# Optimization experiments

Hardware: AMD Instinct MI355X
Metric: run time of the kernel (lower is better)

The kernel has to match this reference:

```python
import jax, jax.numpy as jnp
import numpy as np

NUM_BLOCKS = 8
BLOCK_SIZE = 96  # 768 // 8
LAMBDA = 0.01


def softshrink(x, lam=LAMBDA):
    return jnp.sign(x) * jnp.maximum(jnp.abs(x) - lam, 0.0)


def setup_inputs() -> dict:
    key = jax.random.key(0)
    k1, k2, k3 = jax.random.split(key, 3)
    B, H, W, C = 4, 128, 128, 768
    # xavier_uniform bound for [block_size, block_size] fan_in=fan_out=96
    bound = float(np.sqrt(6.0 / (BLOCK_SIZE + BLOCK_SIZE)))
    x = jax.random.normal(k1, (B, H, W, C), dtype=jnp.float32)
    w1 = jax.random.uniform(k2, (2, NUM_BLOCKS, BLOCK_SIZE, BLOCK_SIZE), minval=-bound, maxval=bound, dtype=jnp.float32)
    w2 = jax.random.uniform(k3, (2, NUM_BLOCKS, BLOCK_SIZE, BLOCK_SIZE), minval=-bound, maxval=bound, dtype=jnp.float32)
    b1 = jnp.zeros((2, NUM_BLOCKS, BLOCK_SIZE), dtype=jnp.float32)
    b2 = jnp.zeros((2, NUM_BLOCKS, BLOCK_SIZE), dtype=jnp.float32)
    return {"x": x, "w1": w1, "w2": w2, "b1": b1, "b2": b2}


def reference(x, w1, w2, b1, b2):
    bias = x
    B, H, W, C = x.shape
    xf = jnp.fft.rfft2(x.astype(jnp.float32), axes=(1, 2), norm='ortho')  # [B,H,W//2+1,C] complex
    Wf = xf.shape[2]
    xf = xf.reshape(B, H, Wf, NUM_BLOCKS, BLOCK_SIZE)
    xr, xi = jnp.real(xf), jnp.imag(xf)
    # first complex block-diagonal MLP layer
    o1r = jnp.einsum('bhwki,kio->bhwko', xr, w1[0]) - jnp.einsum('bhwki,kio->bhwko', xi, w1[1]) + b1[0]
    o1i = jnp.einsum('bhwki,kio->bhwko', xi, w1[0]) + jnp.einsum('bhwki,kio->bhwko', xr, w1[1]) + b1[1]
    o1r = softshrink(o1r)
    o1i = softshrink(o1i)
    # second layer
    o2r = jnp.einsum('bhwki,kio->bhwko', o1r, w2[0]) - jnp.einsum('bhwki,kio->bhwko', o1i, w2[1]) + b2[0]
    o2i = jnp.einsum('bhwki,kio->bhwko', o1i, w2[0]) + jnp.einsum('bhwki,kio->bhwko', o1r, w2[1]) + b2[1]
    o2r = softshrink(o2r)
    o2i = softshrink(o2i)
    yf = (o2r + 1j * o2i).reshape(B, H, Wf, C)
    y = jnp.fft.irfft2(yf, s=(H, W), axes=(1, 2), norm='ortho')
    return y.astype(x.dtype) + bias
```

## Files before the change

kernel.cpp:

```cpp
#include <hip/hip_runtime.h>
#include <cmath>

#define PI_D 3.14159265358979323846

static constexpr int B_ = 4, H_ = 128, W_ = 128, C_ = 768, WF = 65;
static constexpr size_t PLANE = (size_t)B_ * H_ * WF * C_;
static constexpr float LAMBDA_ = 0.01f;

using short8   = __attribute__((ext_vector_type(8))) short;
using floatx16 = __attribute__((ext_vector_type(16))) float;

__device__ __forceinline__ float2 cmul(float2 a, float2 b) {
  return make_float2(a.x * b.x - a.y * b.y, a.x * b.y + a.y * b.x);
}
__device__ __forceinline__ unsigned short f2bfu(float f) {
  union { float f; unsigned u; } v; v.f = f;
  unsigned r = v.u + 0x7FFFu + ((v.u >> 16) & 1u);
  return (unsigned short)(r >> 16);
}
__device__ __forceinline__ float bf2f(unsigned short u) {
  union { unsigned u; float f; } v; v.u = (unsigned)u << 16;
  return v.f;
}
__device__ __forceinline__ float softshrink(float v) {
  return v > LAMBDA_ ? v - LAMBDA_ : (v < -LAMBDA_ ? v + LAMBDA_ : 0.0f);
}

template<int SIGN, int S>
__device__ __forceinline__ void fft64_stage(float2* z, const float2* tw) {
  constexpr int half = 1 << S;
  #pragma unroll
  for (int g = 0; g < 32; ++g) {
    const int j  = g & (half - 1);
    const int i0 = ((g >> S) << (S + 1)) + j;
    const int i1 = i0 + half;
    float2 w = tw[j << (5 - S)];
    if (SIGN > 0) w.y = -w.y;
    float2 t = cmul(w, z[i1]);
    float2 a = z[i0];
    z[i0] = make_float2(a.x + t.x, a.y + t.y);
    z[i1] = make_float2(a.x - t.x, a.y - t.y);
  }
}
template<int SIGN>
__device__ __forceinline__ void fft64(float2* z, const float2* tw) {
  #pragma unroll
  for (int i = 0; i < 64; ++i) {
    const int j = ((i >> 5) & 1) | (((i >> 4) & 1) << 1) | (((i >> 3) & 1) << 2)
                | (((i >> 2) & 1) << 3) | (((i >> 1) & 1) << 4) | ((i & 1) << 5);
    if (i < j) { float2 t = z[i]; z[i] = z[j]; z[j] = t; }
  }
  fft64_stage<SIGN, 0>(z, tw);
  fft64_stage<SIGN, 1>(z, tw);
  fft64_stage<SIGN, 2>(z, tw);
  fft64_stage<SIGN, 3>(z, tw);
  fft64_stage<SIGN, 4>(z, tw);
  fft64_stage<SIGN, 5>(z, tw);
}

__global__ void k_init_tw(float2* tw64, float2* tw128) {
  int t = threadIdx.x;
  if (t < 32) {
    double th = -2.0 * PI_D * (double)t / 64.0;
    tw64[t] = make_float2((float)cos(th), (float)sin(th));
  }
  if (t < 65) {
    double th = -PI_D * (double)t / 64.0;
    tw128[t] = make_float2((float)cos(th), (float)sin(th));
  }
}

__global__ __launch_bounds__(256) void k_wconv(
    const float* __restrict__ w1, const float* __restrict__ w2,
    unsigned short* __restrict__ wbf) {
  const int flat = blockIdx.x * 256 + threadIdx.x;
  const int i  = flat % 104;
  const int t2 = flat / 104;
  const int o  = t2 % 96;
  const int t3 = t2 / 96;
  const int ri = t3 & 1;
  const int t4 = t3 >> 1;
  const int kb = t4 & 7;
  const int layer = t4 >> 3;
  const float* w = layer ? w2 : w1;
  unsigned short v = 0;
  if (i < 96) v = f2bfu(w[((size_t)(ri * 8 + kb) * 96 + i) * 96 + o]);
  wbf[flat] = v;
}

__global__ __launch_bounds__(256) void k_rfft_w(
    const float* __restrict__ x,
    unsigned short* __restrict__ Sr, unsigned short* __restrict__ Si,
    const float2* __restrict__ tw64g, const float2* __restrict__ tw128g) {
  __shared__ float2 stw64[32];
  __shared__ float2 stw128[65];
  const int tid = threadIdx.x;
  if (tid < 32) stw64[tid]  = tw64g[tid];
  if (tid < 65) stw128[tid] = tw128g[tid];
  __syncthreads();
  const int blk = blockIdx.x;
  const int cc = blk % 3, bh = blk / 3;
  const int c = cc * 256 + tid;
  const float* xp = x + (size_t)bh * (W_ * C_) + c;
  float2 z[64];
  #pragma unroll
  for (int n = 0; n < 64; ++n) {
    z[n].x = xp[(size_t)(2 * n) * C_];
    z[n].y = xp[(size_t)(2 * n + 1) * C_];
  }
  fft64<-1>(z, stw64);
  const size_t obase = (size_t)bh * (WF * C_) + c;
  #pragma unroll
  for (int k = 0; k <= 64; ++k) {
    float2 a  = z[k & 63];
    float2 bq = z[(64 - k) & 63];
    float2 ze = make_float2(0.5f * (a.x + bq.x), 0.5f * (a.y - bq.y));
    float2 d  = make_float2(0.5f * (a.x - bq.x), 0.5f * (a.y + bq.y));
    float2 zo = make_float2(d.y, -d.x);
    float2 w  = stw128[k];
    float2 X  = make_float2(ze.x + w.x * zo.x - w.y * zo.y,
                            ze.y + w.x * zo.y + w.y * zo.x);
    Sr[obase + (size_t)k * C_] = f2bfu(X.x);
    Si[obase + (size_t)k * C_] = f2bfu(X.y);
  }
}

template<int SIGN>
__global__ __launch_bounds__(128) void k_fft_h(
    unsigned short* __restrict__ Sr, unsigned short* __restrict__ Si,
    const float2* __restrict__ tw64g, const float2* __restrict__ tw128g) {
  __shared__ float2 stw64[32];
  __shared__ float2 stw128[65];
  __shared__ float2 Elds[64][64];
  const int tid = threadIdx.x;
  if (tid < 32) stw64[tid]  = tw64g[tid];
  if (tid < 65) stw128[tid] = tw128g[tid];
  __syncthreads();
  const int half = tid >> 6, lane = tid & 63;
  const int blk = blockIdx.x;
  const int cc = blk % 12;
  const int t2 = blk / 12;
  const int wf = t2 % 65, b = t2 / 65;
  const int c = cc * 64 + lane;
  const size_t base = ((size_t)b * (H_ * WF) + wf) * C_ + c;
  const size_t hstr = (size_t)WF * C_;
  float2 z[64];
  #pragma unroll
  for (int n = 0; n < 64; ++n) {
    const size_t a = base + (size_t)(2 * n + half) * hstr;
    z[n].x = bf2f(Sr[a]); z[n].y = bf2f(Si[a]);
  }
  fft64<SIGN>(z, stw64);
  if (half == 0) {
    #pragma unroll
    for (int k = 0; k < 64; ++k) Elds[k][lane] = z[k];
  } else {
    #pragma unroll
    for (int k = 0; k < 64; ++k) {
      float2 w = stw128[k];
      if (SIGN > 0) w.y = -w.y;
      z[k] = cmul(w, z[k]);
    }
  }
  __syncthreads();
  if (half == 1) {
    const float scale = (SIGN < 0) ? (1.0f / 128.0f) : 1.0f;
    #pragma unroll
    for (int k = 0; k < 64; ++k) {
      float2 E = Elds[k][lane];
      float2 t = z[k];
      const size_t a0 = base + (size_t)k * hstr;
      const size_t a1 = base + (size_t)(k + 64) * hstr;
      Sr[a0] = f2bfu((E.x + t.x) * scale); Si[a0] = f2bfu((E.y + t.y) * scale);
      Sr[a1] = f2bfu((E.x - t.x) * scale); Si[a1] = f2bfu((E.y - t.y) * scale);
    }
  }
}

__global__ __launch_bounds__(256) void k_mlp(
    unsigned short* __restrict__ Sr, unsigned short* __restrict__ Si,
    const unsigned short* __restrict__ wbf,
    const float* __restrict__ b1, const float* __restrict__ b2) {
  __shared__ __align__(16) unsigned short smem[32768];
  unsigned short* wr   = smem;
  unsigned short* wi   = smem + 9984;
  unsigned short* obuf = smem + 19968;
  const int tid = threadIdx.x;
  const int kb  = blockIdx.x & 7;
  const int p0  = (blockIdx.x >> 3) * 64;
  const int wv  = tid >> 6, lane = tid & 63;
  const int mh = wv & 1, nh = wv >> 1;
  const int n32 = lane & 31, khalf = lane >> 5;

  {
    const unsigned short* g = wbf + (size_t)kb * 19968;
    #pragma unroll
    for (int it = 0; it < 10; ++it) {
      int idx = tid + it * 256;
      if (idx < 2496) *(short8*)&smem[idx * 8] = *(const short8*)&g[idx * 8];
    }
  }
  __syncthreads();

  floatx16 acc[3];
  #pragma unroll
  for (int t = 0; t < 3; ++t)
    #pragma unroll
    for (int e = 0; e < 16; ++e) acc[t][e] = 0.0f;

  const size_t arow = (size_t)(p0 + mh * 32 + n32) * C_ + kb * 96;
  #pragma unroll
  for (int kk = 0; kk < 12; ++kk) {
    const int kr = kk >= 6;
    const int kloc = (kk - kr * 6) * 16 + khalf * 8;
    const unsigned short* ap = (kr ? Si : Sr) + arow + kloc;
    short8 afr = *(const short8*)ap;
    const unsigned short* bb = (kr != nh) ? wi : wr;
    #pragma unroll
    for (int nt = 0; nt < 3; ++nt) {
      short8 bfr = *(const short8*)&bb[(nt * 32 + n32) * 104 + kloc];
      if (kr && !nh) {
        union { short8 s; int v[4]; } u; u.s = bfr;
        u.v[0] ^= 0x80008000; u.v[1] ^= 0x80008000;
        u.v[2] ^= 0x80008000; u.v[3] ^= 0x80008000;
        bfr = u.s;
      }
      acc[nt] = __builtin_amdgcn_mfma_f32_32x32x16_bf16(afr, bfr, acc[nt], 0, 0, 0);
    }
  }

  #pragma unroll
  for (int nt = 0; nt < 3; ++nt) {
    const int o = nt * 32 + n32;
    const float bs = b1[(nh * 8 + kb) * 96 + o];
    const int n = nh * 96 + o;
    #pragma unroll
    for (int reg = 0; reg < 16; ++reg) {
      const int m = mh * 32 + (reg & 3) + 8 * (reg >> 2) + 4 * khalf;
      obuf[m * 200 + n] = f2bfu(softshrink(acc[nt][reg] + bs));
    }
  }
  __syncthreads();

  {
    const unsigned short* g = wbf + (size_t)(8 + kb) * 19968;
    #pragma unroll
    for (int it = 0; it < 10; ++it) {
      int idx = tid + it * 256;
      if (idx < 2496) *(short8*)&smem[idx * 8] = *(const short8*)&g[idx * 8];
    }
  }
  __syncthreads();

  #pragma unroll
  for (int t = 0; t < 3; ++t)
    #pragma unroll
    for (int e = 0; e < 16; ++e) acc[t][e] = 0.0f;

  const int arow2 = (mh * 32 + n32) * 200;
  #pragma unroll
  for (int kk = 0; kk < 12; ++kk) {
    const int kr = kk >= 6;
    const int klocW = (kk - kr * 6) * 16 + khalf * 8;
    short8 afr = *(const short8*)&obuf[arow2 + kk * 16 + khalf * 8];
    const unsigned short* bb = (kr != nh) ? wi : wr;
    #pragma unroll
    for (int nt = 0; nt < 3; ++nt) {
      short8 bfr = *(const short8*)&bb[(nt * 32 + n32) * 104 + klocW];
      if (kr && !nh) {
        union { short8 s; int v[4]; } u; u.s = bfr;
        u.v[0] ^= 0x80008000; u.v[1] ^= 0x80008000;
        u.v[2] ^= 0x80008000; u.v[3] ^= 0x80008000;
        bfr = u.s;
      }
      acc[nt] = __builtin_amdgcn_mfma_f32_32x32x16_bf16(afr, bfr, acc[nt], 0, 0, 0);
    }
  }

  unsigned short* plane = nh ? Si : Sr;
  #pragma unroll
  for (int nt = 0; nt < 3; ++nt) {
    const int o = nt * 32 + n32;
    const float bs = b2[(nh * 8 + kb) * 96 + o];
    #pragma unroll
    for (int reg = 0; reg < 16; ++reg) {
      const int m = mh * 32 + (reg & 3) + 8 * (reg >> 2) + 4 * khalf;
      plane[(size_t)(p0 + m) * C_ + kb * 96 + o] = f2bfu(softshrink(acc[nt][reg] + bs));
    }
  }
}

__global__ __launch_bounds__(256) void k_irfft_w(
    const unsigned short* __restrict__ Sr, const unsigned short* __restrict__ Si,
    const float* __restrict__ xin, float* __restrict__ y,
    const float2* __restrict__ tw64g, const float2* __restrict__ tw128g) {
  __shared__ float2 stw64[32];
  __shared__ float2 stw128[65];
  const int tid = threadIdx.x;
  if (tid < 32) stw64[tid]  = tw64g[tid];
  if (tid < 65) stw128[tid] = tw128g[tid];
  __syncthreads();
  const int blk = blockIdx.x;
  const int cc = blk % 3, bh = blk / 3;
  const int c = cc * 256 + tid;
  const size_t ibase = (size_t)bh * (WF * C_) + c;
  float2 z[64];
  {
    float x0r  = bf2f(Sr[ibase]);
    float x64r = bf2f(Sr[ibase + (size_t)64 * C_]);
    z[0] = make_float2(0.5f * (x0r + x64r), 0.5f * (x0r - x64r));
  }
  #pragma unroll
  for (int k = 1; k <= 32; ++k) {
    float2 a, b;
    a.x = bf2f(Sr[ibase + (size_t)k * C_]);        a.y = bf2f(Si[ibase + (size_t)k * C_]);
    b.x = bf2f(Sr[ibase + (size_t)(64 - k) * C_]); b.y = bf2f(Si[ibase + (size_t)(64 - k) * C_]);
    float2 s = make_float2(0.5f * (a.x + b.x), 0.5f * (a.y - b.y));
    float2 d = make_float2(0.5f * (a.x - b.x), 0.5f * (a.y + b.y));
    float2 w = stw128[k]; w.y = -w.y;
    float2 zo = cmul(w, d);
    z[k] = make_float2(s.x - zo.y, s.y + zo.x);
    if (k < 32) z[64 - k] = make_float2(s.x + zo.y, zo.x - s.y);
  }
  fft64<1>(z, stw64);
  const float* xb = xin + (size_t)bh * (W_ * C_) + c;
  float*       yb = y   + (size_t)bh * (W_ * C_) + c;
  #pragma unroll
  for (int n = 0; n < 64; ++n) {
    yb[(size_t)(2 * n) * C_]     = z[n].x * (1.0f / 64.0f) + xb[(size_t)(2 * n) * C_];
    yb[(size_t)(2 * n + 1) * C_] = z[n].y * (1.0f / 64.0f) + xb[(size_t)(2 * n + 1) * C_];
  }
}

extern "C" void kernel_launch(void* const* d_in, const int* in_sizes, int n_in,
                              void* d_out, int out_size, void* d_ws, size_t ws_size,
                              hipStream_t stream) {
  const float* x  = (const float*)d_in[0];
  const float* w1 = (const float*)d_in[1];
  const float* w2 = (const float*)d_in[2];
  const float* b1 = (const float*)d_in[3];
  const float* b2 = (const float*)d_in[4];
  float* y = (float*)d_out;

  float2* tw64  = (float2*)d_ws;
  float2* tw128 = tw64 + 32;
  unsigned short* wbf = (unsigned short*)((char*)d_ws + 1024);
  unsigned short* Sr  = (unsigned short*)((char*)d_ws + (1 << 20));
  unsigned short* Si  = Sr + PLANE;

  k_init_tw<<<1, 128, 0, stream>>>(tw64, tw128);
  k_wconv<<<dim3(1248), dim3(256), 0, stream>>>(w1, w2, wbf);
  k_rfft_w<<<dim3(B_ * H_ * 3), dim3(256), 0, stream>>>(x, Sr, Si, tw64, tw128);
  k_fft_h<-1><<<dim3(B_ * WF * 12), dim3(128), 0, stream>>>(Sr, Si, tw64, tw128);
  k_mlp<<<dim3(520 * 8), dim3(256), 0, stream>>>(Sr, Si, wbf, b1, b2);
  k_fft_h<1><<<dim3(B_ * WF * 12), dim3(128), 0, stream>>>(Sr, Si, tw64, tw128);
  k_irfft_w<<<dim3(B_ * H_ * 3), dim3(256), 0, stream>>>(Sr, Si, x, y, tw64, tw128);
}
```

Measured before the change: 824.2 us.

## Fuse H-axis FFT, block MLP, and inverse H-FFT into one LDS-resident kernel

Replaces the separate forward H-FFT, MLP, and inverse H-FFT kernels with a single kernel. Each block loads a full 128-row column tile for one (b, wf, channel-block) into LDS, does the FFT along H, both MLP layers with MFMA, and the inverse FFT, then writes back once. The goal is to cut two full round trips of the bf16 spectrum planes through global memory. In exchange each block uses about 144KB of dynamic LDS, which limits occupancy, and a quarter of threads sit idle during the FFT phases because only 96 of 128 channel lanes are active.

Result: faster. 776.0 us (-5.8%).

```diff
diff --git a/kernel.cpp b/kernel.cpp
--- a/kernel.cpp
+++ b/kernel.cpp
@@ -125,167 +125,209 @@
   }
 }
 
-template<int SIGN>
-__global__ __launch_bounds__(128) void k_fft_h(
+static constexpr int L_W = 512, L_P = 20480, L_S = 47104;
+static constexpr int L_BYTES = 73728 * 2;
+
+__global__ __launch_bounds__(256) void k_mid(
     unsigned short* __restrict__ Sr, unsigned short* __restrict__ Si,
+    const unsigned short* __restrict__ wbf,
+    const float* __restrict__ b1, const float* __restrict__ b2,
     const float2* __restrict__ tw64g, const float2* __restrict__ tw128g) {
-  __shared__ float2 stw64[32];
-  __shared__ float2 stw128[65];
-  __shared__ float2 Elds[64][64];
+  extern __shared__ unsigned short lds[];
+  float2* stw64  = (float2*)lds;
+  float2* stw128 = (float2*)(lds + 128);
   const int tid = threadIdx.x;
   if (tid < 32) stw64[tid]  = tw64g[tid];
   if (tid < 65) stw128[tid] = tw128g[tid];
-  __syncthreads();
-  const int half = tid >> 6, lane = tid & 63;
-  const int blk = blockIdx.x;
-  const int cc = blk % 12;
-  const int t2 = blk / 12;
+
+  const int kb = blockIdx.x & 7;
+  const int t2 = blockIdx.x >> 3;
   const int wf = t2 % 65, b = t2 / 65;
-  const int c = cc * 64 + lane;
-  const size_t base = ((size_t)b * (H_ * WF) + wf) * C_ + c;
   const size_t hstr = (size_t)WF * C_;
+  const size_t gb0  = ((size_t)b * H_ * WF + wf) * (size_t)C_ + (size_t)kb * 96;
+
+  {
+    const unsigned short* g = wbf + (size_t)kb * 19968;
+    #pragma unroll
+    for (int it = 0; it < 10; ++it) {
+      int idx = tid + it * 256;
+      if (idx < 2496) *(short8*)&lds[L_W + idx * 8] = *(const short8*)&g[idx * 8];
+    }
+  }
+  #pragma unroll
+  for (int it = 0; it < 48; ++it) {
+    const int u = it * 256 + tid;
+    const int p = (it >= 24);
+    const int v = u - p * 6144;
+    const int row = v / 48, cp = v - row * 48;
+    const unsigned short* src = (p ? Si : Sr) + gb0 + (size_t)row * hstr + cp * 2;
+    *(unsigned int*)&lds[L_P + p * 13312 + row * 104 + cp * 2] =
+        *(const unsigned int*)src;
+  }
+  __syncthreads();
+
+  const int wv = tid >> 6, lane = tid & 63;
+  const int half = wv >> 1;
+  const int ch = tid & 127;
+  const bool act = ch < 96;
+  float2* Efd = (float2*)&lds[L_S];
+
   float2 z[64];
-  #pragma unroll
-  for (int n = 0; n < 64; ++n) {
-    const size_t a = base + (size_t)(2 * n + half) * hstr;
-    z[n].x = bf2f(Sr[a]); z[n].y = bf2f(Si[a]);
-  }
-  fft64<SIGN>(z, stw64);
-  if (half == 0) {
-    #pragma unroll
-    for (int k = 0; k < 64; ++k) Elds[k][lane] = z[k];
-  } else {
+  if (act) {
+    #pragma unroll
+    for (int n = 0; n < 64; ++n) {
+      const int row = 2 * n + half;
+      z[n].x = bf2f(lds[L_P + row * 104 + ch]);
+      z[n].y = bf2f(lds[L_P + 13312 + row * 104 + ch]);
+    }
+    fft64<-1>(z, stw64);
+    if (half == 0) {
+      #pragma unroll
+      for (int k = 0; k < 64; ++k) Efd[k * 96 + ch] = z[k];
+    } else {
+      #pragma unroll
+      for (int k = 0; k < 64; ++k) z[k] = cmul(stw128[k], z[k]);
+    }
+  }
+  __syncthreads();
+  if (act && half == 1) {
+    const float sc = 1.0f / 128.0f;
     #pragma unroll
     for (int k = 0; k < 64; ++k) {
-      float2 w = stw128[k];
-      if (SIGN > 0) w.y = -w.y;
-      z[k] = cmul(w, z[k]);
-    }
-  }
-  __syncthreads();
-  if (half == 1) {
-    const float scale = (SIGN < 0) ? (1.0f / 128.0f) : 1.0f;
-    #pragma unroll
-    for (int k = 0; k < 64; ++k) {
-      float2 E = Elds[k][lane];
-      float2 t = z[k];
-      const size_t a0 = base + (size_t)k * hstr;
-      const size_t a1 = base + (size_t)(k + 64) * hstr;
-      Sr[a0] = f2bfu((E.x + t.x) * scale); Si[a0] = f2bfu((E.y + t.y) * scale);
-      Sr[a1] = f2bfu((E.x - t.x) * scale); Si[a1] = f2bfu((E.y - t.y) * scale);
-    }
-  }
-}
-
-__global__ __launch_bounds__(256) void k_mlp(
-    unsigned short* __restrict__ Sr, unsigned short* __restrict__ Si,
-    const unsigned short* __restrict__ wbf,
-    const float* __restrict__ b1, const float* __restrict__ b2) {
-  __shared__ __align__(16) unsigned short smem[32768];
-  unsigned short* wr   = smem;
-  unsigned short* wi   = smem + 9984;
-  unsigned short* obuf = smem + 19968;
-  const int tid = threadIdx.x;
-  const int kb  = blockIdx.x & 7;
-  const int p0  = (blockIdx.x >> 3) * 64;
-  const int wv  = tid >> 6, lane = tid & 63;
+      const float2 E = Efd[k * 96 + ch];
+      const float2 t = z[k];
+      lds[L_P + k * 104 + ch]                 = f2bfu((E.x + t.x) * sc);
+      lds[L_P + 13312 + k * 104 + ch]         = f2bfu((E.y + t.y) * sc);
+      lds[L_P + (k + 64) * 104 + ch]          = f2bfu((E.x - t.x) * sc);
+      lds[L_P + 13312 + (k + 64) * 104 + ch]  = f2bfu((E.y - t.y) * sc);
+    }
+  }
+  __syncthreads();
+
   const int mh = wv & 1, nh = wv >> 1;
   const int n32 = lane & 31, khalf = lane >> 5;
+  const unsigned short* wr = lds + L_W;
+  const unsigned short* wi = lds + L_W + 9984;
+
+  #pragma unroll
+  for (int mt = 0; mt < 2; ++mt) {
+    const int p0 = mt * 64;
+    floatx16 acc[3];
+    #pragma unroll
+    for (int t = 0; t < 3; ++t)
+      #pragma unroll
+      for (int e = 0; e < 16; ++e) acc[t][e] = 0.0f;
+    const int arow = p0 + mh * 32 + n32;
+    #pragma unroll
+    for (int kk = 0; kk < 12; ++kk) {
+      const int kr = kk >= 6;
+      const int kloc = (kk - kr * 6) * 16 + khalf * 8;
+      short8 afr = *(const short8*)&lds[L_P + kr * 13312 + arow * 104 + kloc];
+      const unsigned short* bb = (kr != nh) ? wi : wr;
+      #pragma unroll
+      for (int nt = 0; nt < 3; ++nt) {
+        short8 bfr = *(const short8*)&bb[(nt * 32 + n32) * 104 + kloc];
+        if (kr && !nh) {
+          union { short8 s; int v[4]; } u; u.s = bfr;
+          u.v[0] ^= 0x80008000; u.v[1] ^= 0x80008000;
+          u.v[2] ^= 0x80008000; u.v[3] ^= 0x80008000;
+          bfr = u.s;
+        }
+        acc[nt] = __builtin_amdgcn_mfma_f32_32x32x16_bf16(afr, bfr, acc[nt], 0, 0, 0);
+      }
+    }
+    #pragma unroll
+    for (int nt = 0; nt < 3; ++nt) {
+      const int o = nt * 32 + n32;
+      const float bs = b1[(nh * 8 + kb) * 96 + o];
+      #pragma unroll
+      for (int reg = 0; reg < 16; ++reg) {
+        const int m = p0 + mh * 32 + (reg & 3) + 8 * (reg >> 2) + 4 * khalf;
+        lds[L_S + nh * 13312 + m * 104 + o] = f2bfu(softshrink(acc[nt][reg] + bs));
+      }
+    }
+  }
+  __syncthreads();
 
   {
-    const unsigned short* g = wbf + (size_t)kb * 19968;
+    const unsigned short* g = wbf + (size_t)(8 + kb) * 19968;
     #pragma unroll
     for (int it = 0; it < 10; ++it) {
       int idx = tid + it * 256;
-      if (idx < 2496) *(short8*)&smem[idx * 8] = *(const short8*)&g[idx * 8];
-    }
-  }
-  __syncthreads();
-
-  floatx16 acc[3];
-  #pragma unroll
-  for (int t = 0; t < 3; ++t)
-    #pragma unroll
-    for (int e = 0; e < 16; ++e) acc[t][e] = 0.0f;
-
-  const size_t arow = (size_t)(p0 + mh * 32 + n32) * C_ + kb * 96;
-  #pragma unroll
-  for (int kk = 0; kk < 12; ++kk) {
-    const int kr = kk >= 6;
-    const int kloc = (kk - kr * 6) * 16 + khalf * 8;
-    const unsigned short* ap = (kr ? Si : Sr) + arow + kloc;
-    short8 afr = *(const short8*)ap;
-    const unsigned short* bb = (kr != nh) ? wi : wr;
+      if (idx < 2496) *(short8*)&lds[L_W + idx * 8] = *(const short8*)&g[idx * 8];
+    }
+  }
+  __syncthreads();
+
+  #pragma unroll
+  for (int mt = 0; mt < 2; ++mt) {
+    const int p0 = mt * 64;
+    floatx16 acc[3];
+    #pragma unroll
+    for (int t = 0; t < 3; ++t)
+      #pragma unroll
+      for (int e = 0; e < 16; ++e) acc[t][e] = 0.0f;
+    const int arow = p0 + mh * 32 + n32;
+    #pragma unroll
+    for (int kk = 0; kk < 12; ++kk) {
+      const int kr = kk >= 6;
+      const int kloc = (kk - kr * 6) * 16 + khalf * 8;
+      short8 afr = *(const short8*)&lds[L_S + kr * 13312 + arow * 104 + kloc];
+      const unsigned short* bb = (kr != nh) ? wi : wr;
+      #pragma unroll
+      for (int nt = 0; nt < 3; ++nt) {
+        short8 bfr = *(const short8*)&bb[(nt * 32 + n32) * 104 + kloc];
+        if (kr && !nh) {
+          union { short8 s; int v[4]; } u; u.s = bfr;
+          u.v[0] ^= 0x80008000; u.v[1] ^= 0x80008000;
+          u.v[2] ^= 0x80008000; u.v[3] ^= 0x80008000;
+          bfr = u.s;
+        }
+        acc[nt] = __builtin_amdgcn_mfma_f32_32x32x16_bf16(afr, bfr, acc[nt], 0, 0, 0);
+      }
+    }
     #pragma unroll
     for (int nt = 0; nt < 3; ++nt) {
-      short8 bfr = *(const short8*)&bb[(nt * 32 + n32) * 104 + kloc];
-      if (kr && !nh) {
-        union { short8 s; int v[4]; } u; u.s = bfr;
-        u.v[0] ^= 0x80008000; u.v[1] ^= 0x80008000;
-        u.v[2] ^= 0x80008000; u.v[3] ^= 0x80008000;
-        bfr = u.s;
+      const int o = nt * 32 + n32;
+      const float bs = b2[(nh * 8 + kb) * 96 + o];
+      #pragma unroll
+      for (int reg = 0; reg < 16; ++reg) {
+        const int m = p0 + mh * 32 + (reg & 3) + 8 * (reg >> 2) + 4 * khalf;
+        lds[L_P + nh * 13312 + m * 104 + o] = f2bfu(softshrink(acc[nt][reg] + bs));
       }
-      acc[nt] = __builtin_amdgcn_mfma_f32_32x32x16_bf16(afr, bfr, acc[nt], 0, 0, 0);
-    }
-  }
-
-  #pragma unroll
-  for (int nt = 0; nt < 3; ++nt) {
-    const int o = nt * 32 + n32;
-    const float bs = b1[(nh * 8 + kb) * 96 + o];
-    const int n = nh * 96 + o;
-    #pragma unroll
-    for (int reg = 0; reg < 16; ++reg) {
-      const int m = mh * 32 + (reg & 3) + 8 * (reg >> 2) + 4 * khalf;
-      obuf[m * 200 + n] = f2bfu(softshrink(acc[nt][reg] + bs));
-    }
-  }
-  __syncthreads();
-
-  {
-    const unsigned short* g = wbf + (size_t)(8 + kb) * 19968;
-    #pragma unroll
-    for (int it = 0; it < 10; ++it) {
-      int idx = tid + it * 256;
-      if (idx < 2496) *(short8*)&smem[idx * 8] = *(const short8*)&g[idx * 8];
-    }
-  }
-  __syncthreads();
-
-  #pragma unroll
-  for (int t = 0; t < 3; ++t)
-    #pragma unroll
-    for (int e = 0; e < 16; ++e) acc[t][e] = 0.0f;
-
-  const int arow2 = (mh * 32 + n32) * 200;
-  #pragma unroll
-  for (int kk = 0; kk < 12; ++kk) {
-    const int kr = kk >= 6;
-    const int klocW = (kk - kr * 6) * 16 + khalf * 8;
-    short8 afr = *(const short8*)&obuf[arow2 + kk * 16 + khalf * 8];
-    const unsigned short* bb = (kr != nh) ? wi : wr;
-    #pragma unroll
-    for (int nt = 0; nt < 3; ++nt) {
-      short8 bfr = *(const short8*)&bb[(nt * 32 + n32) * 104 + klocW];
-      if (kr && !nh) {
-        union { short8 s; int v[4]; } u; u.s = bfr;
-        u.v[0] ^= 0x80008000; u.v[1] ^= 0x80008000;
-        u.v[2] ^= 0x80008000; u.v[3] ^= 0x80008000;
-        bfr = u.s;
+    }
+  }
+  __syncthreads();
+
+  if (act) {
+    #pragma unroll
+    for (int n = 0; n < 64; ++n) {
+      const int row = 2 * n + half;
+      z[n].x = bf2f(lds[L_P + row * 104 + ch]);
+      z[n].y = bf2f(lds[L_P + 13312 + row * 104 + ch]);
+    }
+    fft64<1>(z, stw64);
+    if (half == 0) {
+      #pragma unroll
+      for (int k = 0; k < 64; ++k) Efd[k * 96 + ch] = z[k];
+    } else {
+      #pragma unroll
+      for (int k = 0; k < 64; ++k) {
+        float2 w = stw128[k]; w.y = -w.y;
+        z[k] = cmul(w, z[k]);
       }
-      acc[nt] = __builtin_amdgcn_mfma_f32_32x32x16_bf16(afr, bfr, acc[nt], 0, 0, 0);
-    }
-  }
-
-  unsigned short* plane = nh ? Si : Sr;
-  #pragma unroll
-  for (int nt = 0; nt < 3; ++nt) {
-    const int o = nt * 32 + n32;
-    const float bs = b2[(nh * 8 + kb) * 96 + o];
-    #pragma unroll
-    for (int reg = 0; reg < 16; ++reg) {
-      const int m = mh * 32 + (reg & 3) + 8 * (reg >> 2) + 4 * khalf;
-      plane[(size_t)(p0 + m) * C_ + kb * 96 + o] = f2bfu(softshrink(acc[nt][reg] + bs));
+    }
+  }
+  __syncthreads();
+  if (act && half == 1) {
+    #pragma unroll
+    for (int k = 0; k < 64; ++k) {
+      const float2 E = Efd[k * 96 + ch];
+      const float2 t = z[k];
+      const size_t g0 = gb0 + (size_t)k * hstr + ch;
+      const size_t g1 = gb0 + (size_t)(k + 64) * hstr + ch;
+      Sr[g0] = f2bfu(E.x + t.x); Si[g0] = f2bfu(E.y + t.y);
+      Sr[g1] = f2bfu(E.x - t.x); Si[g1] = f2bfu(E.y - t.y);
     }
   }
 }
@@ -348,11 +390,16 @@
   unsigned short* Sr  = (unsigned short*)((char*)d_ws + (1 << 20));
   unsigned short* Si  = Sr + PLANE;
 
+  static bool attr_done = false;
+  if (!attr_done) {
+    hipFuncSetAttribute((const void*)k_mid,
+                        hipFuncAttributeMaxDynamicSharedMemorySize, L_BYTES);
+    attr_done = true;
+  }
+
   k_init_tw<<<1, 128, 0, stream>>>(tw64, tw128);
   k_wconv<<<dim3(1248), dim3(256), 0, stream>>>(w1, w2, wbf);
   k_rfft_w<<<dim3(B_ * H_ * 3), dim3(256), 0, stream>>>(x, Sr, Si, tw64, tw128);
-  k_fft_h<-1><<<dim3(B_ * WF * 12), dim3(128), 0, stream>>>(Sr, Si, tw64, tw128);
-  k_mlp<<<dim3(520 * 8), dim3(256), 0, stream>>>(Sr, Si, wbf, b1, b2);
-  k_fft_h<1><<<dim3(B_ * WF * 12), dim3(128), 0, stream>>>(Sr, Si, tw64, tw128);
+  k_mid<<<dim3(260 * 8), dim3(256), L_BYTES, stream>>>(Sr, Si, wbf, b1, b2, tw64, tw128);
   k_irfft_w<<<dim3(B_ * H_ * 3), dim3(256), 0, stream>>>(Sr, Si, x, y, tw64, tw128);
 }
```
